# Optimization experiments

Hardware: AMD Instinct MI355X
Metric: run time of the kernel (lower is better)

Reference implementation:

```python
import jax, jax.numpy as jnp
import numpy as np

B, S, D, H, V = 4, 1024, 2048, 16, 32000
LAYERS, DFF, HID, NSENT, NLAB = 2, 8192, 100, 3, 3
HD = D // H
LN2 = 0.6931471805599453


def _ln(x, g, b):
    m = jnp.mean(x, axis=-1, keepdims=True)
    v = jnp.mean((x - m) ** 2, axis=-1, keepdims=True)
    return (x - m) * jax.lax.rsqrt(v + 1e-5) * g + b


def setup_inputs():
    key = jax.random.key(0)
    ks = jax.random.split(key, 12)
    s = 0.02
    return dict(
        input_ids=jax.random.randint(ks[0], (B, S), 0, V),
        attention_mask=jnp.ones((B, S), dtype=jnp.int32),
        sentiment=jax.random.normal(ks[1], (B, NSENT), dtype=jnp.float32),
        perplexity=jax.random.uniform(ks[2], (B,), dtype=jnp.float32) + 1.0,
        emb=jax.random.normal(ks[3], (V, D), dtype=jnp.float32) * s,
        ln1_g=jnp.ones((LAYERS, D)), ln1_b=jnp.zeros((LAYERS, D)),
        qkv_w=jax.random.normal(ks[4], (LAYERS, D, 3 * D), dtype=jnp.float32) * s,
        wo_w=jax.random.normal(ks[5], (LAYERS, D, D), dtype=jnp.float32) * s,
        ln2_g=jnp.ones((LAYERS, D)), ln2_b=jnp.zeros((LAYERS, D)),
        w1=jax.random.normal(ks[6], (LAYERS, D, DFF), dtype=jnp.float32) * s,
        w2=jax.random.normal(ks[7], (LAYERS, DFF, D), dtype=jnp.float32) * s,
        lnf_g=jnp.ones((D,)), lnf_b=jnp.zeros((D,)),
        head_w=jax.random.normal(ks[8], (D, V), dtype=jnp.float32) * s,
        red_w=jax.random.normal(ks[9], (D, HID), dtype=jnp.float32) * s,
        red_b=jnp.zeros((HID,)),
        cls_w=jax.random.normal(ks[10], (HID + NSENT + 2, NLAB), dtype=jnp.float32) * s,
        cls_b=jnp.zeros((NLAB,)),
    )


def _lm(input_ids, attention_mask, emb, ln1_g, ln1_b, qkv_w, wo_w, ln2_g, ln2_b, w1, w2, lnf_g, lnf_b, head_w):
    x = emb[input_ids]  # [B,S,D]
    amask = attention_mask.astype(jnp.float32)
    causal = jnp.tril(jnp.ones((S, S), dtype=bool))
    bias = jnp.where(causal[None, None, :, :] & (amask[:, None, None, :] > 0), 0.0, -1e9)
    for l in range(LAYERS):
        h = _ln(x, ln1_g[l], ln1_b[l])
        qkv = h @ qkv_w[l]  # [B,S,3D]
        q, k, v = [t.reshape(B, S, H, HD) for t in jnp.split(qkv, 3, axis=-1)]
        scores = jnp.einsum('bqhd,bkhd->bhqk', q, k) / np.float32(np.sqrt(HD)) + bias
        attn = jax.nn.softmax(scores, axis=-1)
        o = jnp.einsum('bhqk,bkhd->bqhd', attn, v).reshape(B, S, D)
        x = x + o @ wo_w[l]
        h = _ln(x, ln2_g[l], ln2_b[l])
        x = x + jax.nn.gelu(h @ w1[l]) @ w2[l]
    h = _ln(x, lnf_g, lnf_b)
    logits = h @ head_w  # [B,S,V]
    return h, logits


def reference(input_ids, attention_mask, sentiment, perplexity, emb, ln1_g, ln1_b, qkv_w, wo_w, ln2_g, ln2_b, w1, w2, lnf_g, lnf_b, head_w, red_w, red_b, cls_w, cls_b):
    h, logits = _lm(input_ids, attention_mask, emb, ln1_g, ln1_b, qkv_w, wo_w,
                    ln2_g, ln2_b, w1, w2, lnf_g, lnf_b, head_w)
    amask = attention_mask.astype(jnp.float32)
    pooled = jnp.mean(h, axis=1)  # mean over seq -> [B,D]
    # probs = softmax(logits).detach(); gather own token prob; -log2(p)
    lg = jax.lax.stop_gradient(logits)
    logZ = jax.scipy.special.logsumexp(lg, axis=-1)  # [B,S]
    tok_logit = jnp.take_along_axis(lg, input_ids[..., None], axis=-1)[..., 0]
    subword_surp = -(tok_logit - logZ) / LN2 * amask
    mean_surprisal = subword_surp.sum(axis=1) / amask.sum(axis=1)  # [B]
    r = jax.nn.leaky_relu(pooled @ red_w + red_b)  # torch intent: LeakyReLU after reducer
    feats = jnp.concatenate([r, sentiment, perplexity[:, None], mean_surprisal[:, None]], axis=1)
    return feats @ cls_w + cls_b  # [B, NLAB]
```

## Files before the change

kernel.cpp:

```cpp
#include <hip/hip_runtime.h>

typedef unsigned short u16;
typedef __bf16 bf16x8 __attribute__((ext_vector_type(8)));
typedef float f32x4 __attribute__((ext_vector_type(4)));

__device__ __forceinline__ u16 f2bf(float f){
  unsigned u = __float_as_uint(f);
  unsigned r = u + 0x7FFFu + ((u >> 16) & 1u);
  return (u16)(r >> 16);
}
__device__ __forceinline__ float bf2f(u16 v){ return __uint_as_float(((unsigned)v) << 16); }

__device__ __forceinline__ void gload16(const void* g, void* l){
  __builtin_amdgcn_global_load_lds(
      (const __attribute__((address_space(1))) unsigned int*)g,
      (__attribute__((address_space(3))) unsigned int*)l, 16, 0, 0);
}

__global__ __launch_bounds__(256) void transp_k(const float* __restrict__ in, u16* __restrict__ out, int K, int N)
{
  __shared__ float tl[64][65];
  const int n0 = blockIdx.x * 64, k0 = blockIdx.y * 64;
  const int t = threadIdx.x;
  const int r = t >> 4, c4 = t & 15;
#pragma unroll
  for (int i = 0; i < 4; ++i){
    float4 v = *(const float4*)(in + (size_t)(k0 + r + i*16) * N + n0 + c4*4);
    tl[r + i*16][c4*4 + 0] = v.x; tl[r + i*16][c4*4 + 1] = v.y;
    tl[r + i*16][c4*4 + 2] = v.z; tl[r + i*16][c4*4 + 3] = v.w;
  }
  __syncthreads();
#pragma unroll
  for (int i = 0; i < 4; ++i){
    const int n = r + i*16;
    ushort4 o;
    o.x = f2bf(tl[c4*4 + 0][n]); o.y = f2bf(tl[c4*4 + 1][n]);
    o.z = f2bf(tl[c4*4 + 2][n]); o.w = f2bf(tl[c4*4 + 3][n]);
    *(ushort4*)(out + (size_t)(n0 + n) * K + k0 + c4*4) = o;
  }
}

__global__ __launch_bounds__(256) void embed_k(const int* __restrict__ ids, const float* __restrict__ emb, float* __restrict__ x)
{
  const int row = blockIdx.x;
  const int c = blockIdx.y * 256 + threadIdx.x;
  x[(size_t)row * 2048 + c] = emb[(size_t)ids[row] * 2048 + c];
}

__global__ __launch_bounds__(256) void ln_k(const float* __restrict__ x, const float* __restrict__ gw,
                                            const float* __restrict__ bw, u16* __restrict__ o)
{
  const int row = blockIdx.x, t = threadIdx.x;
  const int lane = t & 63, wid = t >> 6;
  const float4* xr = (const float4*)(x + (size_t)row * 2048);
  float4 v1 = xr[t], v2 = xr[t + 256];
  float s1 = v1.x + v1.y + v1.z + v1.w + v2.x + v2.y + v2.z + v2.w;
  float s2 = v1.x*v1.x + v1.y*v1.y + v1.z*v1.z + v1.w*v1.w
           + v2.x*v2.x + v2.y*v2.y + v2.z*v2.z + v2.w*v2.w;
#pragma unroll
  for (int off = 32; off >= 1; off >>= 1){ s1 += __shfl_down(s1, off); s2 += __shfl_down(s2, off); }
  __shared__ float rb[2][4];
  __shared__ float mv[2];
  if (lane == 0){ rb[0][wid] = s1; rb[1][wid] = s2; }
  __syncthreads();
  if (t == 0){
    float a = rb[0][0] + rb[0][1] + rb[0][2] + rb[0][3];
    float q = rb[1][0] + rb[1][1] + rb[1][2] + rb[1][3];
    float mean = a * (1.f/2048.f);
    float var  = q * (1.f/2048.f) - mean*mean;
    mv[0] = mean; mv[1] = rsqrtf(var + 1e-5f);
  }
  __syncthreads();
  const float mean = mv[0], rstd = mv[1];
  const float4* g4 = (const float4*)gw;
  const float4* b4 = (const float4*)bw;
  float4 ga = g4[t], ba = b4[t], gb = g4[t + 256], bb2 = b4[t + 256];
  ushort4 o1, o2;
  o1.x = f2bf((v1.x - mean)*rstd*ga.x + ba.x);
  o1.y = f2bf((v1.y - mean)*rstd*ga.y + ba.y);
  o1.z = f2bf((v1.z - mean)*rstd*ga.z + ba.z);
  o1.w = f2bf((v1.w - mean)*rstd*ga.w + ba.w);
  o2.x = f2bf((v2.x - mean)*rstd*gb.x + bb2.x);
  o2.y = f2bf((v2.y - mean)*rstd*gb.y + bb2.y);
  o2.z = f2bf((v2.z - mean)*rstd*gb.z + bb2.z);
  o2.w = f2bf((v2.w - mean)*rstd*gb.w + bb2.w);
  ((ushort4*)(o + (size_t)row * 2048))[t] = o1;
  ((ushort4*)(o + (size_t)row * 2048))[t + 256] = o2;
}

enum { M_QKV = 0, M_RES = 1, M_GELU = 2, M_LSE = 3 };

template<int MODE, int BM>
__global__ __launch_bounds__(512, 2) void gemm2_k(
    const u16* __restrict__ A, const u16* __restrict__ BT,
    int N, int K, int MB,
    u16* __restrict__ outb, float* __restrict__ outf,
    float* __restrict__ partial, float* __restrict__ tokl,
    const int* __restrict__ ids, u16* __restrict__ vtout)
{
  constexpr int BK  = 32;
  constexpr int ASZ = BM * BK;
  constexpr int BSZ = 256 * BK;
  constexpr int BUF = ASZ + BSZ;
  constexpr int NFR = BM / 32;
  __shared__ u16 lds[3 * BUF];

  const int tid  = threadIdx.x;
  const int wv   = tid >> 6, lane = tid & 63;
  const int wr   = wv >> 2,  wc   = wv & 3;
  const int lg   = lane >> 4, lr  = lane & 15;

  const int nwg = gridDim.x;
  const int bid = blockIdx.x;
  const int swz = ((nwg & 7) == 0) ? ((bid & 7) * (nwg >> 3) + (bid >> 3)) : bid;
  const int bm = swz % MB, bn = swz / MB;
  const int m0 = bm * BM, n0 = bn * 256;

  const int ll = lane >> 3;
  const int cc = lane & 7;
  const int lc = cc ^ ll;
  const int gr = (ll << 1) + (lc >> 2);
  const int gk = (lc & 3) << 3;

  const u16* gA = A  + (size_t)m0 * K + gk;
  const u16* gB = BT + (size_t)n0 * K + gk;

  f32x4 acc[NFR][4];
#pragma unroll
  for (int i = 0; i < NFR; ++i)
#pragma unroll
    for (int j = 0; j < 4; ++j)
#pragma unroll
      for (int r = 0; r < 4; ++r) acc[i][j][r] = 0.f;

  const int nt = K >> 5;

  auto STAGE = [&](int bi, int kt){
    char* bA = (char*)lds + (size_t)bi * BUF * 2;
    char* bB = bA + ASZ * 2;
    const size_t ko = (size_t)kt * 32;
    if constexpr (BM == 256){
      gload16(gA + (size_t)((wv    ) * 16 + gr) * K + ko, bA + (wv    ) * 1024);
      gload16(gA + (size_t)((wv + 8) * 16 + gr) * K + ko, bA + (wv + 8) * 1024);
    } else {
      gload16(gA + (size_t)(wv * 16 + gr) * K + ko, bA + wv * 1024);
    }
    gload16(gB + (size_t)((wv    ) * 16 + gr) * K + ko, bB + (wv    ) * 1024);
    gload16(gB + (size_t)((wv + 8) * 16 + gr) * K + ko, bB + (wv + 8) * 1024);
  };

  STAGE(0, 0);
  STAGE(1, 1);

  for (int t = 0; t < nt; ++t){
    if (t + 1 < nt){
      if constexpr (BM == 256) asm volatile("s_waitcnt vmcnt(4) lgkmcnt(0)" ::: "memory");
      else                     asm volatile("s_waitcnt vmcnt(3) lgkmcnt(0)" ::: "memory");
    } else {
      asm volatile("s_waitcnt vmcnt(0) lgkmcnt(0)" ::: "memory");
    }
    __builtin_amdgcn_s_barrier();
    if (t + 2 < nt) STAGE((t + 2) % 3, t + 2);

    const char* bA = (const char*)lds + (size_t)(t % 3) * BUF * 2;
    const char* bB = bA + ASZ * 2;
    bf16x8 af[NFR], bq[4];
#pragma unroll
    for (int i = 0; i < NFR; ++i){
      const int ra = wr * (BM / 2) + i * 16 + lr;
      const int p = ra >> 1;
      const int slot = (((ra & 1) << 2) | lg) ^ (p & 7);
      af[i] = *(const bf16x8*)(bA + p * 128 + slot * 16);
    }
#pragma unroll
    for (int j = 0; j < 4; ++j){
      const int rb = wc * 64 + j * 16 + lr;
      const int p = rb >> 1;
      const int slot = (((rb & 1) << 2) | lg) ^ (p & 7);
      bq[j] = *(const bf16x8*)(bB + p * 128 + slot * 16);
    }
    __builtin_amdgcn_s_setprio(1);
#pragma unroll
    for (int i = 0; i < NFR; ++i)
#pragma unroll
      for (int j = 0; j < 4; ++j)
        acc[i][j] = __builtin_amdgcn_mfma_f32_16x16x32_bf16(af[i], bq[j], acc[i][j], 0, 0, 0);
    __builtin_amdgcn_s_setprio(0);
  }

#pragma unroll
  for (int i = 0; i < NFR; ++i){
#pragma unroll
    for (int r = 0; r < 4; ++r){
      const int row = m0 + wr * (BM / 2) + i * 16 + lg * 4 + r;
      if constexpr (MODE == M_LSE){
        const int id = ids[row];
        float esum = 0.f;
#pragma unroll
        for (int j = 0; j < 4; ++j){
          const int col = n0 + wc * 64 + j * 16 + lr;
          const float v = acc[i][j][r];
          if (col == id) tokl[row] = v;
          esum += __expf(v);
        }
#pragma unroll
        for (int off = 8; off >= 1; off >>= 1) esum += __shfl_xor(esum, off);
        if (lr == 0) partial[(size_t)row * 500 + bn * 4 + wc] = esum;
      } else {
#pragma unroll
        for (int j = 0; j < 4; ++j){
          const int col = n0 + wc * 64 + j * 16 + lr;
          const float v = acc[i][j][r];
          if constexpr (MODE == M_RES){
            float* pp = outf + (size_t)row * N + col;
            *pp += v;
          } else if constexpr (MODE == M_GELU){
            float u = 0.7978845608028654f * (v + 0.044715f * v * v * v);
            u = fminf(fmaxf(u, -15.f), 15.f);
            const float ex = __expf(2.f * u);
            const float th = (ex - 1.f) / (ex + 1.f);
            outb[(size_t)row * N + col] = f2bf(0.5f * v * (1.f + th));
          } else {
            const u16 uv = f2bf(v);
            if (col < 4096) outb[(size_t)row * 6144 + col] = uv;
            else {
              int dd2 = col - 4096;
              const int hh = dd2 >> 7; dd2 &= 127;
              vtout[(((size_t)((row >> 10) * 16 + hh)) * 128 + dd2) * 1024 + (row & 1023)] = uv;
            }
          }
        }
      }
    }
  }
}

__global__ __launch_bounds__(64) void attn_k(const u16* __restrict__ qkv, const u16* __restrict__ vT, u16* __restrict__ o16)
{
  __shared__ u16 P[16 * 40];
  const int bid = blockIdx.x;
  const int qt = bid & 63, bh = bid >> 6;
  const int h = bh & 15, b = bh >> 4;
  const int lane = threadIdx.x, lg = lane >> 4, lr = lane & 15;
  const int q0 = qt << 4;
  const u16* qrow  = qkv + (size_t)(b * 1024 + q0 + lr) * 6144 + h * 128;
  const u16* krow  = qkv + (size_t)(b * 1024 + lr) * 6144 + 2048 + h * 128;
  const u16* vbase = vT + (size_t)(b * 16 + h) * 128 * 1024;

  bf16x8 qf[4];
#pragma unroll
  for (int c = 0; c < 4; ++c) qf[c] = *(const bf16x8*)(qrow + c * 32 + lg * 8);

  float m[4], l[4];
  f32x4 oacc[8];
#pragma unroll
  for (int r = 0; r < 4; ++r){ m[r] = -1e30f; l[r] = 0.f; }
#pragma unroll
  for (int f = 0; f < 8; ++f)
#pragma unroll
    for (int r = 0; r < 4; ++r) oacc[f][r] = 0.f;

  const float scale = 0.08838834764831845f;
  const int nk2 = (qt >> 1) + 1;
  for (int k2 = 0; k2 < nk2; ++k2){
    float e[2][4];
    float rmax[4];
#pragma unroll
    for (int r = 0; r < 4; ++r) rmax[r] = -1e30f;
#pragma unroll
    for (int hh = 0; hh < 2; ++hh){
      const int kt = k2 * 2 + hh;
      if (kt <= qt){
        f32x4 s;
#pragma unroll
        for (int r = 0; r < 4; ++r) s[r] = 0.f;
#pragma unroll
        for (int c = 0; c < 4; ++c){
          bf16x8 kf = *(const bf16x8*)(krow + (size_t)(kt * 16) * 6144 + c * 32 + lg * 8);
          s = __builtin_amdgcn_mfma_f32_16x16x32_bf16(qf[c], kf, s, 0, 0, 0);
        }
#pragma unroll
        for (int r = 0; r < 4; ++r){
          float sv = s[r] * scale;
          if (kt * 16 + lr > q0 + lg * 4 + r) sv = -1e30f;
          e[hh][r] = sv;
          rmax[r] = fmaxf(rmax[r], sv);
        }
      } else {
#pragma unroll
        for (int r = 0; r < 4; ++r) e[hh][r] = -1e30f;
      }
    }
#pragma unroll
    for (int off = 8; off >= 1; off >>= 1)
#pragma unroll
      for (int r = 0; r < 4; ++r) rmax[r] = fmaxf(rmax[r], __shfl_xor(rmax[r], off));
    float corr[4], rsum[4];
#pragma unroll
    for (int r = 0; r < 4; ++r){
      const float mn = fmaxf(m[r], rmax[r]);
      corr[r] = __expf(m[r] - mn);
      m[r] = mn;
      const float e0 = __expf(e[0][r] - mn);
      const float e1 = __expf(e[1][r] - mn);
      e[0][r] = e0; e[1][r] = e1;
      rsum[r] = e0 + e1;
    }
#pragma unroll
    for (int off = 8; off >= 1; off >>= 1)
#pragma unroll
      for (int r = 0; r < 4; ++r) rsum[r] += __shfl_xor(rsum[r], off);
#pragma unroll
    for (int r = 0; r < 4; ++r) l[r] = l[r] * corr[r] + rsum[r];
#pragma unroll
    for (int hh = 0; hh < 2; ++hh)
#pragma unroll
      for (int r = 0; r < 4; ++r)
        P[(lg * 4 + r) * 40 + hh * 16 + lr] = f2bf(e[hh][r]);
#pragma unroll
    for (int f = 0; f < 8; ++f)
#pragma unroll
      for (int r = 0; r < 4; ++r) oacc[f][r] = oacc[f][r] * corr[r];
    __syncthreads();
    const bf16x8 pa = *(const bf16x8*)((const u16*)P + lr * 40 + lg * 8);
#pragma unroll
    for (int f = 0; f < 8; ++f){
      bf16x8 vb = *(const bf16x8*)(vbase + (size_t)(f * 16 + lr) * 1024 + k2 * 32 + lg * 8);
      oacc[f] = __builtin_amdgcn_mfma_f32_16x16x32_bf16(pa, vb, oacc[f], 0, 0, 0);
    }
    __syncthreads();
  }
  u16* orow = o16 + (size_t)(b * 1024 + q0 + lg * 4) * 2048 + h * 128;
#pragma unroll
  for (int r = 0; r < 4; ++r){
    const float linv = 1.0f / l[r];
#pragma unroll
    for (int f = 0; f < 8; ++f)
      orow[(size_t)r * 2048 + f * 16 + lr] = f2bf(oacc[f][r] * linv);
  }
}

__global__ __launch_bounds__(256) void lse_k(const float* __restrict__ partial, const float* __restrict__ tokl,
                                             const int* __restrict__ amask, float* __restrict__ surp)
{
  const int row = blockIdx.x, t = threadIdx.x, lane = t & 63, wid = t >> 6;
  float s = 0.f;
  if (t < 250) s = partial[(size_t)row * 500 + t] + partial[(size_t)row * 500 + t + 250];
#pragma unroll
  for (int off = 32; off >= 1; off >>= 1) s += __shfl_down(s, off);
  __shared__ float rb[4];
  if (lane == 0) rb[wid] = s;
  __syncthreads();
  if (t == 0){
    const float tot = rb[0] + rb[1] + rb[2] + rb[3];
    surp[row] = (logf(tot) - tokl[row]) * 1.4426950408889634f * (float)amask[row];
  }
}

__global__ __launch_bounds__(256) void pool_k(const u16* __restrict__ h16, float* __restrict__ pooled)
{
  const int d = blockIdx.x * 256 + threadIdx.x;
  const int b = blockIdx.y;
  const u16* p = h16 + (size_t)b * 1024 * 2048 + d;
  float a0 = 0.f, a1 = 0.f, a2 = 0.f, a3 = 0.f;
  for (int s = 0; s < 1024; s += 4){
    a0 += bf2f(p[(size_t)(s + 0) * 2048]);
    a1 += bf2f(p[(size_t)(s + 1) * 2048]);
    a2 += bf2f(p[(size_t)(s + 2) * 2048]);
    a3 += bf2f(p[(size_t)(s + 3) * 2048]);
  }
  pooled[b * 2048 + d] = (a0 + a1 + a2 + a3) * (1.f / 1024.f);
}

__global__ __launch_bounds__(256) void cls_k(const float* __restrict__ pooled, const float* __restrict__ surp,
                                             const int* __restrict__ amask, const float* __restrict__ sent,
                                             const float* __restrict__ ppl, const float* __restrict__ redw,
                                             const float* __restrict__ redb, const float* __restrict__ clsw,
                                             const float* __restrict__ clsb, float* __restrict__ out)
{
  const int b = blockIdx.x, t = threadIdx.x;
  const int lane = t & 63, wid = t >> 6;
  __shared__ float pl[2048];
  __shared__ float feats[112];
  __shared__ float rbuf[2][4];
#pragma unroll
  for (int i = 0; i < 8; ++i) pl[t + i * 256] = pooled[b * 2048 + t + i * 256];
  float ssum = 0.f, msum = 0.f;
#pragma unroll
  for (int i = 0; i < 4; ++i){
    const int s = t + i * 256;
    ssum += surp[b * 1024 + s];
    msum += (float)amask[b * 1024 + s];
  }
#pragma unroll
  for (int off = 32; off >= 1; off >>= 1){ ssum += __shfl_down(ssum, off); msum += __shfl_down(msum, off); }
  if (lane == 0){ rbuf[0][wid] = ssum; rbuf[1][wid] = msum; }
  __syncthreads();
  if (t == 0){
    float a = 0.f, c = 0.f;
    for (int i = 0; i < 4; ++i){ a += rbuf[0][i]; c += rbuf[1][i]; }
    feats[104] = a / c;
  }
  if (t >= 100 && t < 103) feats[t] = sent[b * 3 + (t - 100)];
  if (t == 103) feats[103] = ppl[b];
  if (t < 100){
    float a = redb[t];
    for (int d = 0; d < 2048; ++d) a += pl[d] * redw[d * 100 + t];
    feats[t] = (a > 0.f) ? a : 0.01f * a;
  }
  __syncthreads();
  if (t < 3){
    float a = clsb[t];
    for (int i = 0; i < 105; ++i) a += feats[i] * clsw[i * 3 + t];
    out[b * 3 + t] = a;
  }
}

extern "C" void kernel_launch(void* const* d_in, const int* in_sizes, int n_in,
                              void* d_out, int out_size, void* d_ws, size_t ws_size,
                              hipStream_t stream)
{
  (void)in_sizes; (void)n_in; (void)out_size; (void)ws_size;
  const int*   ids   = (const int*)d_in[0];
  const int*   amask = (const int*)d_in[1];
  const float* sent  = (const float*)d_in[2];
  const float* ppl   = (const float*)d_in[3];
  const float* emb   = (const float*)d_in[4];
  const float* ln1g  = (const float*)d_in[5];
  const float* ln1b  = (const float*)d_in[6];
  const float* qkvw  = (const float*)d_in[7];
  const float* wow   = (const float*)d_in[8];
  const float* ln2g  = (const float*)d_in[9];
  const float* ln2b  = (const float*)d_in[10];
  const float* w1    = (const float*)d_in[11];
  const float* w2    = (const float*)d_in[12];
  const float* lnfg  = (const float*)d_in[13];
  const float* lnfb  = (const float*)d_in[14];
  const float* headw = (const float*)d_in[15];
  const float* redw  = (const float*)d_in[16];
  const float* redb  = (const float*)d_in[17];
  const float* clsw  = (const float*)d_in[18];
  const float* clsb  = (const float*)d_in[19];
  float* out = (float*)d_out;

  char* p = (char*)d_ws;
  u16* wqkvT = (u16*)p; p += (size_t)2 * 6144 * 2048 * 2;
  u16* woT   = (u16*)p; p += (size_t)2 * 2048 * 2048 * 2;
  u16* w1T   = (u16*)p; p += (size_t)2 * 8192 * 2048 * 2;
  u16* w2T   = (u16*)p; p += (size_t)2 * 2048 * 8192 * 2;
  u16* whT   = (u16*)p; p += (size_t)32000 * 2048 * 2;
  float* xbuf = (float*)p; p += (size_t)4096 * 2048 * 4;
  u16* h16   = (u16*)p; p += (size_t)4096 * 2048 * 2;
  u16* qkv16 = (u16*)p;
  u16* vT16  = (u16*)(p + (size_t)4096 * 6144 * 2);
  u16* ffn16 = (u16*)p;
  p += (size_t)4096 * 6144 * 2 + (size_t)4096 * 2048 * 2;
  u16* o16   = (u16*)p; p += (size_t)4096 * 2048 * 2;
  float* partial = (float*)p; p += (size_t)4096 * 500 * 4;
  float* tokl = (float*)p; p += (size_t)4096 * 4;
  float* surp = (float*)p; p += (size_t)4096 * 4;
  float* pooled = (float*)p; p += (size_t)4 * 2048 * 4;

  for (int l = 0; l < 2; ++l){
    transp_k<<<dim3(6144/64, 2048/64), 256, 0, stream>>>(qkvw + (size_t)l*2048*6144, wqkvT + (size_t)l*6144*2048, 2048, 6144);
    transp_k<<<dim3(2048/64, 2048/64), 256, 0, stream>>>(wow  + (size_t)l*2048*2048, woT   + (size_t)l*2048*2048, 2048, 2048);
    transp_k<<<dim3(8192/64, 2048/64), 256, 0, stream>>>(w1   + (size_t)l*2048*8192, w1T   + (size_t)l*8192*2048, 2048, 8192);
    transp_k<<<dim3(2048/64, 8192/64), 256, 0, stream>>>(w2   + (size_t)l*8192*2048, w2T   + (size_t)l*2048*8192, 8192, 2048);
  }
  transp_k<<<dim3(32000/64, 2048/64), 256, 0, stream>>>(headw, whT, 2048, 32000);

  embed_k<<<dim3(4096, 8), 256, 0, stream>>>(ids, emb, xbuf);

  for (int l = 0; l < 2; ++l){
    ln_k<<<4096, 256, 0, stream>>>(xbuf, ln1g + l*2048, ln1b + l*2048, h16);
    gemm2_k<M_QKV,256><<<16*24, 512, 0, stream>>>(h16, wqkvT + (size_t)l*6144*2048, 6144, 2048, 16,
                                                  qkv16, nullptr, nullptr, nullptr, nullptr, vT16);
    attn_k<<<4096, 64, 0, stream>>>(qkv16, vT16, o16);
    gemm2_k<M_RES,128><<<32*8, 512, 0, stream>>>(o16, woT + (size_t)l*2048*2048, 2048, 2048, 32,
                                                 nullptr, xbuf, nullptr, nullptr, nullptr, nullptr);
    ln_k<<<4096, 256, 0, stream>>>(xbuf, ln2g + l*2048, ln2b + l*2048, h16);
    gemm2_k<M_GELU,256><<<16*32, 512, 0, stream>>>(h16, w1T + (size_t)l*8192*2048, 8192, 2048, 16,
                                                   ffn16, nullptr, nullptr, nullptr, nullptr, nullptr);
    gemm2_k<M_RES,128><<<32*8, 512, 0, stream>>>(ffn16, w2T + (size_t)l*2048*8192, 2048, 8192, 32,
                                                 nullptr, xbuf, nullptr, nullptr, nullptr, nullptr);
  }
  ln_k<<<4096, 256, 0, stream>>>(xbuf, lnfg, lnfb, h16);
  gemm2_k<M_LSE,256><<<16*125, 512, 0, stream>>>(h16, whT, 32000, 2048, 16,
                                                 nullptr, nullptr, partial, tokl, ids, nullptr);
  lse_k<<<4096, 256, 0, stream>>>(partial, tokl, amask, surp);
  pool_k<<<dim3(8, 4), 256, 0, stream>>>(h16, pooled);
  cls_k<<<4, 256, 0, stream>>>(pooled, surp, amask, sent, ppl, redw, redb, clsw, clsb, out);
}
```

Baseline: 2.416 ms.

## Add 256x256 GEMM kernel with split-K-half LDS pipeline for large GEMMs

Introduces gemm6_k, a 256x256-tile bf16 MFMA GEMM that stages A and B in 32-wide K halves into double-buffered LDS. Global-to-LDS loads for later tiles are interleaved between four MFMA phases, separated by barriers and priority bumps. It replaces gemm2_k for the QKV, FFN-up (GELU) and LM-head (LSE) GEMMs, and the QKV epilogue now writes V transposed as 4-element vector stores. The aim is to hide load latency and raise MFMA utilisation, at the cost of higher register pressure and many barriers per K step.

```diff
diff --git a/kernel.cpp b/kernel.cpp
--- a/kernel.cpp
+++ b/kernel.cpp
@@ -193,7 +193,160 @@
 #pragma unroll
     for (int r = 0; r < 4; ++r){
       const int row = m0 + wr * (BM / 2) + i * 16 + lg * 4 + r;
-      if constexpr (MODE == M_LSE){
+#pragma unroll
+      for (int j = 0; j < 4; ++j){
+        const int col = n0 + wc * 64 + j * 16 + lr;
+        const float v = acc[i][j][r];
+        if constexpr (MODE == M_RES){
+          float* pp = outf + (size_t)row * N + col;
+          *pp += v;
+        } else if constexpr (MODE == M_GELU){
+          float u = 0.7978845608028654f * (v + 0.044715f * v * v * v);
+          u = fminf(fmaxf(u, -15.f), 15.f);
+          const float ex = __expf(2.f * u);
+          const float th = (ex - 1.f) / (ex + 1.f);
+          outb[(size_t)row * N + col] = f2bf(0.5f * v * (1.f + th));
+        }
+      }
+    }
+  }
+}
+
+template<int MODE>
+__global__ __launch_bounds__(512, 2) void gemm6_k(
+    const u16* __restrict__ A, const u16* __restrict__ BT,
+    int N, int K, int MB,
+    u16* __restrict__ outb, float* __restrict__ outf,
+    float* __restrict__ partial, float* __restrict__ tokl,
+    const int* __restrict__ ids, u16* __restrict__ vtout)
+{
+  __shared__ u16 lds[65536];
+
+  const int tid  = threadIdx.x;
+  const int wv   = tid >> 6, lane = tid & 63;
+  const int wr   = wv >> 2,  wc   = wv & 3;
+  const int lg   = lane >> 4, lr  = lane & 15;
+
+  const int nwg = gridDim.x;
+  const int bid = blockIdx.x;
+  const int swz = ((nwg & 7) == 0) ? ((bid & 7) * (nwg >> 3) + (bid >> 3)) : bid;
+  const int bm = swz % MB, bn = swz / MB;
+  const int m0 = bm * 256, n0 = bn * 256;
+
+  const int ll = lane >> 3;
+  const int cc = lane & 7;
+  const int lc = cc ^ ll;
+  const int gr = (ll << 1) + (lc >> 2);
+  const int gk = (lc & 3) << 3;
+
+  const u16* gA = A  + (size_t)m0 * K + gk;
+  const u16* gB = BT + (size_t)n0 * K + gk;
+
+  f32x4 acc[8][4];
+#pragma unroll
+  for (int i = 0; i < 8; ++i)
+#pragma unroll
+    for (int j = 0; j < 4; ++j)
+#pragma unroll
+      for (int r = 0; r < 4; ++r) acc[i][j][r] = 0.f;
+
+  const int nt = K >> 6;
+
+  auto RB = [&](int tt, int kh, int bsel) -> char* {
+    return (char*)lds + (((tt & 1) << 16) | (kh << 15) | (bsel << 14));
+  };
+  auto STG = [&](const u16* gsrc, int tt, int kh, int bsel){
+    char* dst = RB(tt, kh, bsel);
+    const size_t ko = (size_t)tt * 64 + kh * 32;
+    gload16(gsrc + (size_t)((wv    ) * 16 + gr) * K + ko, dst + (wv    ) * 1024);
+    gload16(gsrc + (size_t)((wv + 8) * 16 + gr) * K + ko, dst + (wv + 8) * 1024);
+  };
+  auto FRG = [&](int tt, int kh, int bsel, int row) -> bf16x8 {
+    const int p = row >> 1;
+    const int slot = (((row & 1) << 2) | lg) ^ (p & 7);
+    return *(const bf16x8*)(RB(tt, kh, bsel) + p * 128 + slot * 16);
+  };
+
+  STG(gA, 0, 0, 0); STG(gB, 0, 0, 1);
+  STG(gA, 0, 1, 0); STG(gB, 0, 1, 1);
+  STG(gA, 1, 0, 0); STG(gB, 1, 0, 1);
+  asm volatile("s_waitcnt vmcnt(4)" ::: "memory");
+  __builtin_amdgcn_s_barrier();
+
+  for (int u = 0; u < nt; ++u){
+    bf16x8 bq[4], aa[4];
+#pragma unroll
+    for (int j = 0; j < 4; ++j) bq[j] = FRG(u, 0, 1, wc * 64 + j * 16 + lr);
+#pragma unroll
+    for (int i = 0; i < 4; ++i) aa[i] = FRG(u, 0, 0, wr * 128 + i * 16 + lr);
+    if (u + 1 < nt) STG(gA, u + 1, 1, 0);
+    __builtin_amdgcn_s_barrier();
+    asm volatile("s_waitcnt lgkmcnt(0)" ::: "memory");
+    __builtin_amdgcn_s_setprio(1);
+#pragma unroll
+    for (int i = 0; i < 4; ++i)
+#pragma unroll
+      for (int j = 0; j < 4; ++j)
+        acc[i][j] = __builtin_amdgcn_mfma_f32_16x16x32_bf16(aa[i], bq[j], acc[i][j], 0, 0, 0);
+    __builtin_amdgcn_s_setprio(0);
+    __builtin_amdgcn_s_barrier();
+
+    bf16x8 ab[4];
+#pragma unroll
+    for (int i = 0; i < 4; ++i) ab[i] = FRG(u, 0, 0, wr * 128 + (4 + i) * 16 + lr);
+    if (u + 1 < nt) STG(gB, u + 1, 1, 1);
+    __builtin_amdgcn_s_barrier();
+    asm volatile("s_waitcnt lgkmcnt(0)" ::: "memory");
+    __builtin_amdgcn_s_setprio(1);
+#pragma unroll
+    for (int i = 0; i < 4; ++i)
+#pragma unroll
+      for (int j = 0; j < 4; ++j)
+        acc[4 + i][j] = __builtin_amdgcn_mfma_f32_16x16x32_bf16(ab[i], bq[j], acc[4 + i][j], 0, 0, 0);
+    __builtin_amdgcn_s_setprio(0);
+    __builtin_amdgcn_s_barrier();
+
+    bf16x8 bq2[4], ac[4];
+#pragma unroll
+    for (int j = 0; j < 4; ++j) bq2[j] = FRG(u, 1, 1, wc * 64 + j * 16 + lr);
+#pragma unroll
+    for (int i = 0; i < 4; ++i) ac[i] = FRG(u, 1, 0, wr * 128 + i * 16 + lr);
+    if (u + 2 < nt) STG(gA, u + 2, 0, 0);
+    __builtin_amdgcn_s_barrier();
+    asm volatile("s_waitcnt lgkmcnt(0)" ::: "memory");
+    __builtin_amdgcn_s_setprio(1);
+#pragma unroll
+    for (int i = 0; i < 4; ++i)
+#pragma unroll
+      for (int j = 0; j < 4; ++j)
+        acc[i][j] = __builtin_amdgcn_mfma_f32_16x16x32_bf16(ac[i], bq2[j], acc[i][j], 0, 0, 0);
+    __builtin_amdgcn_s_setprio(0);
+    __builtin_amdgcn_s_barrier();
+
+    bf16x8 ad[4];
+#pragma unroll
+    for (int i = 0; i < 4; ++i) ad[i] = FRG(u, 1, 0, wr * 128 + (4 + i) * 16 + lr);
+    if (u + 2 < nt) STG(gB, u + 2, 0, 1);
+    if (u + 2 < nt)      asm volatile("s_waitcnt vmcnt(4)" ::: "memory");
+    else if (u + 1 < nt) asm volatile("s_waitcnt vmcnt(0)" ::: "memory");
+    __builtin_amdgcn_s_barrier();
+    asm volatile("s_waitcnt lgkmcnt(0)" ::: "memory");
+    __builtin_amdgcn_s_setprio(1);
+#pragma unroll
+    for (int i = 0; i < 4; ++i)
+#pragma unroll
+      for (int j = 0; j < 4; ++j)
+        acc[4 + i][j] = __builtin_amdgcn_mfma_f32_16x16x32_bf16(ad[i], bq2[j], acc[4 + i][j], 0, 0, 0);
+    __builtin_amdgcn_s_setprio(0);
+    __builtin_amdgcn_s_barrier();
+  }
+
+#pragma unroll
+  for (int i = 0; i < 8; ++i){
+    if constexpr (MODE == M_LSE){
+#pragma unroll
+      for (int r = 0; r < 4; ++r){
+        const int row = m0 + wr * 128 + i * 16 + lg * 4 + r;
         const int id = ids[row];
         float esum = 0.f;
 #pragma unroll
@@ -206,7 +359,32 @@
 #pragma unroll
         for (int off = 8; off >= 1; off >>= 1) esum += __shfl_xor(esum, off);
         if (lr == 0) partial[(size_t)row * 500 + bn * 4 + wc] = esum;
-      } else {
+      }
+    } else if constexpr (MODE == M_QKV){
+#pragma unroll
+      for (int j = 0; j < 4; ++j){
+        const int colb = n0 + wc * 64 + j * 16;
+        if (colb < 4096){
+#pragma unroll
+          for (int r = 0; r < 4; ++r){
+            const int row = m0 + wr * 128 + i * 16 + lg * 4 + r;
+            outb[(size_t)row * 6144 + colb + lr] = f2bf(acc[i][j][r]);
+          }
+        } else {
+          const int srow = m0 + wr * 128 + i * 16 + lg * 4;
+          const int b = srow >> 10, s = srow & 1023;
+          int dd = colb + lr - 4096;
+          const int hh = dd >> 7; dd &= 127;
+          ushort4 o;
+          o.x = f2bf(acc[i][j][0]); o.y = f2bf(acc[i][j][1]);
+          o.z = f2bf(acc[i][j][2]); o.w = f2bf(acc[i][j][3]);
+          *(ushort4*)(vtout + ((size_t)(b * 16 + hh) * 128 + dd) * 1024 + s) = o;
+        }
+      }
+    } else {
+#pragma unroll
+      for (int r = 0; r < 4; ++r){
+        const int row = m0 + wr * 128 + i * 16 + lg * 4 + r;
 #pragma unroll
         for (int j = 0; j < 4; ++j){
           const int col = n0 + wc * 64 + j * 16 + lr;
@@ -214,20 +392,12 @@
           if constexpr (MODE == M_RES){
             float* pp = outf + (size_t)row * N + col;
             *pp += v;
-          } else if constexpr (MODE == M_GELU){
-            float u = 0.7978845608028654f * (v + 0.044715f * v * v * v);
-            u = fminf(fmaxf(u, -15.f), 15.f);
-            const float ex = __expf(2.f * u);
+          } else {
+            float u2 = 0.7978845608028654f * (v + 0.044715f * v * v * v);
+            u2 = fminf(fmaxf(u2, -15.f), 15.f);
+            const float ex = __expf(2.f * u2);
             const float th = (ex - 1.f) / (ex + 1.f);
             outb[(size_t)row * N + col] = f2bf(0.5f * v * (1.f + th));
-          } else {
-            const u16 uv = f2bf(v);
-            if (col < 4096) outb[(size_t)row * 6144 + col] = uv;
-            else {
-              int dd2 = col - 4096;
-              const int hh = dd2 >> 7; dd2 &= 127;
-              vtout[(((size_t)((row >> 10) * 16 + hh)) * 128 + dd2) * 1024 + (row & 1023)] = uv;
-            }
           }
         }
       }
@@ -473,20 +643,20 @@
 
   for (int l = 0; l < 2; ++l){
     ln_k<<<4096, 256, 0, stream>>>(xbuf, ln1g + l*2048, ln1b + l*2048, h16);
-    gemm2_k<M_QKV,256><<<16*24, 512, 0, stream>>>(h16, wqkvT + (size_t)l*6144*2048, 6144, 2048, 16,
-                                                  qkv16, nullptr, nullptr, nullptr, nullptr, vT16);
+    gemm6_k<M_QKV><<<16*24, 512, 0, stream>>>(h16, wqkvT + (size_t)l*6144*2048, 6144, 2048, 16,
+                                              qkv16, nullptr, nullptr, nullptr, nullptr, vT16);
     attn_k<<<4096, 64, 0, stream>>>(qkv16, vT16, o16);
     gemm2_k<M_RES,128><<<32*8, 512, 0, stream>>>(o16, woT + (size_t)l*2048*2048, 2048, 2048, 32,
                                                  nullptr, xbuf, nullptr, nullptr, nullptr, nullptr);
     ln_k<<<4096, 256, 0, stream>>>(xbuf, ln2g + l*2048, ln2b + l*2048, h16);
-    gemm2_k<M_GELU,256><<<16*32, 512, 0, stream>>>(h16, w1T + (size_t)l*8192*2048, 8192, 2048, 16,
-                                                   ffn16, nullptr, nullptr, nullptr, nullptr, nullptr);
+    gemm6_k<M_GELU><<<16*32, 512, 0, stream>>>(h16, w1T + (size_t)l*8192*2048, 8192, 2048, 16,
+                                               ffn16, nullptr, nullptr, nullptr, nullptr, nullptr);
     gemm2_k<M_RES,128><<<32*8, 512, 0, stream>>>(ffn16, w2T + (size_t)l*2048*8192, 2048, 8192, 32,
                                                  nullptr, xbuf, nullptr, nullptr, nullptr, nullptr);
   }
   ln_k<<<4096, 256, 0, stream>>>(xbuf, lnfg, lnfb, h16);
-  gemm2_k<M_LSE,256><<<16*125, 512, 0, stream>>>(h16, whT, 32000, 2048, 16,
-                                                 nullptr, nullptr, partial, tokl, ids, nullptr);
+  gemm6_k<M_LSE><<<16*125, 512, 0, stream>>>(h16, whT, 32000, 2048, 16,
+                                             nullptr, nullptr, partial, tokl, ids, nullptr);
   lse_k<<<4096, 256, 0, stream>>>(partial, tokl, amask, surp);
   pool_k<<<dim3(8, 4), 256, 0, stream>>>(h16, pooled);
   cls_k<<<4, 256, 0, stream>>>(pooled, surp, amask, sent, ppl, redw, redb, clsw, clsb, out);
```

Result: faster. 2.340 ms (-3.2%).
